# Kernel tuning notes

Hardware: AMD Instinct MI355X
Metric: run time of the kernel (lower is better)

The kernel has to match this reference:

```python
import jax, jax.numpy as jnp
import numpy as np

N = 50000
EPS = 1e-5


def gcn_conv(x, W, b, src, dst, n):
    # x: [n, Cin]; W: [Cin, Cout]; src/dst: [E+n] with self-loops included
    h = x @ W  # dense GEMM
    deg = jax.ops.segment_sum(jnp.ones_like(dst, dtype=h.dtype), dst, num_segments=n)
    dinv = jnp.where(deg > 0, jax.lax.rsqrt(deg), 0.0)
    norm = dinv[src] * dinv[dst]  # [E+n]
    msgs = h[src] * norm[:, None]  # gather + scale
    out = jax.ops.segment_sum(msgs, dst, num_segments=n)  # scatter-add
    return out + b


def batch_norm(x, gamma, beta, mean, var):
    return (x - mean) * jax.lax.rsqrt(var + EPS) * gamma + beta


def setup_inputs() -> dict:
    key = jax.random.key(0)
    ks = jax.random.split(key, 16)
    IN, H, OUT, E = 1280, 256, 500, 1600000
    x = jax.random.normal(ks[0], (N, IN), dtype=jnp.float32)
    edge_index = jax.random.randint(ks[1], (2, E), 0, N, dtype=jnp.int64)
    def lin(k, cin, cout):
        return jax.random.normal(k, (cin, cout), dtype=jnp.float32) / np.sqrt(cin)
    return {
        "x": x,
        "edge_index": edge_index,
        "W1": lin(ks[2], IN, H), "b1": jnp.zeros((H,), jnp.float32),
        "g1": jnp.ones((H,), jnp.float32), "be1": jnp.zeros((H,), jnp.float32),
        "m1": 0.1 * jax.random.normal(ks[3], (H,), jnp.float32),
        "v1": 0.5 + jax.random.uniform(ks[4], (H,), jnp.float32),
        "W2": lin(ks[5], H, H), "b2": jnp.zeros((H,), jnp.float32),
        "g2": jnp.ones((H,), jnp.float32), "be2": jnp.zeros((H,), jnp.float32),
        "m2": 0.1 * jax.random.normal(ks[6], (H,), jnp.float32),
        "v2": 0.5 + jax.random.uniform(ks[7], (H,), jnp.float32),
        "W3": lin(ks[8], H, OUT), "b3": jnp.zeros((OUT,), jnp.float32),
    }


def reference(x, edge_index, W1, b1, g1, be1, m1, v1, W2, b2, g2, be2, m2, v2, W3, b3):
    n = x.shape[0]
    loops = jnp.arange(n, dtype=edge_index.dtype)
    src = jnp.concatenate([edge_index[0], loops])
    dst = jnp.concatenate([edge_index[1], loops])
    h = gcn_conv(x, W1, b1, src, dst, n)
    h = jax.nn.relu(batch_norm(h, g1, be1, m1, v1))
    h = gcn_conv(h, W2, b2, src, dst, n)
    h = jax.nn.relu(batch_norm(h, g2, be2, m2, v2))
    return gcn_conv(h, W3, b3, src, dst, n)
```

## Files before the change

### kernel.cpp

```cpp
#include <hip/hip_runtime.h>
#include <hip/hip_bf16.h>
#include <stdint.h>

typedef __attribute__((ext_vector_type(4))) float f32x4;
typedef __attribute__((ext_vector_type(8))) short s16x8;
typedef __attribute__((ext_vector_type(4))) unsigned short u16x4;

#define EPSBN 1e-5f

__device__ __forceinline__ float bf2f(unsigned short u) {
  union { unsigned int i; float f; } w; w.i = ((unsigned int)u) << 16; return w.f;
}
__device__ __forceinline__ unsigned short f2bf(float f) {
  __hip_bfloat16 h = __float2bfloat16(f);
  unsigned short u; __builtin_memcpy(&u, &h, 2); return u;
}
__device__ __forceinline__ void gld_lds16(const void* g, void* l) {
  __builtin_amdgcn_global_load_lds(
      (const __attribute__((address_space(1))) void*)(g),
      (__attribute__((address_space(3))) void*)(l), 16, 0, 0);
}

__global__ void k_count(const int* __restrict__ dst, unsigned* __restrict__ deg, int E) {
  int i = blockIdx.x * 256 + threadIdx.x;
  if (i < E) atomicAdd(&deg[dst[i]], 1u);
}
__global__ void k_prep2(const unsigned* __restrict__ deg, float* __restrict__ dinv,
                        unsigned* __restrict__ bsum, int n) {
  __shared__ unsigned s[256];
  int t = threadIdx.x, i = blockIdx.x * 256 + t;
  unsigned d = (i < n) ? deg[i] + 1u : 0u;
  if (i < n) dinv[i] = rsqrtf((float)d);
  s[t] = d;
  __syncthreads();
  for (int st = 128; st > 0; st >>= 1) {
    if (t < st) s[t] += s[t + st];
    __syncthreads();
  }
  if (t == 0) bsum[blockIdx.x] = s[0];
}
__global__ void k_scan_top(const unsigned* __restrict__ bsum, unsigned* __restrict__ bpre,
                           int nb, unsigned* __restrict__ offs, int n) {
  __shared__ unsigned s[256];
  int t = threadIdx.x;
  unsigned v = (t < nb) ? bsum[t] : 0u;
  s[t] = v; __syncthreads();
  for (int d = 1; d < 256; d <<= 1) {
    unsigned a = (t >= d) ? s[t - d] : 0u;
    __syncthreads();
    s[t] += a;
    __syncthreads();
  }
  bpre[t] = s[t] - v;
  if (t == 255) offs[n] = s[255];
}
__global__ void k_scan_fin(const unsigned* __restrict__ deg, const unsigned* __restrict__ bpre,
                           unsigned* __restrict__ offs, unsigned* __restrict__ cur, int n) {
  __shared__ unsigned s[256];
  int t = threadIdx.x, i = blockIdx.x * 256 + t;
  unsigned v = (i < n) ? deg[i] + 1u : 0u;
  s[t] = v; __syncthreads();
  for (int d = 1; d < 256; d <<= 1) {
    unsigned a = (t >= d) ? s[t - d] : 0u;
    __syncthreads();
    s[t] += a;
    __syncthreads();
  }
  if (i < n) {
    unsigned o = bpre[blockIdx.x] + s[t] - v;
    offs[i] = o; cur[i] = o;
  }
}
__global__ void k_fill(const int* __restrict__ src, const int* __restrict__ dst,
                       unsigned* __restrict__ cur, unsigned short* __restrict__ ewp,
                       int E, int n) {
  int i = blockIdx.x * 256 + threadIdx.x;
  int s, d;
  if (i < E)          { s = src[i]; d = dst[i]; }
  else if (i < E + n) { s = d = i - E; }
  else return;
  unsigned p = atomicAdd(&cur[d], 1u);
  ewp[p] = (unsigned short)s;
}
__global__ __launch_bounds__(256) void k_sortw(const unsigned* __restrict__ offs,
                                               unsigned short* __restrict__ ewp, int nN) {
  int wv = (blockIdx.x * 256 + threadIdx.x) >> 6;
  int lane = threadIdx.x & 63;
  if (wv >= nN) return;
  unsigned beg = offs[wv], end = offs[wv + 1];
  int len = (int)(end - beg);
  if (len > 64) return;
  int k = (lane < len) ? (int)ewp[beg + lane] : 0x10000;
#pragma unroll
  for (int size = 2; size <= 64; size <<= 1) {
#pragma unroll
    for (int stride = size >> 1; stride > 0; stride >>= 1) {
      int other = __shfl_xor(k, stride);
      bool up = (lane & size) == 0;
      bool lower = (lane & stride) == 0;
      k = (lower == up) ? min(k, other) : max(k, other);
    }
  }
  if (lane < len) ewp[beg + lane] = (unsigned short)k;
}
__global__ void k_wt3(const float* __restrict__ W1, unsigned short* __restrict__ Wt1,
                      const float* __restrict__ W2, unsigned short* __restrict__ Wt2,
                      const float* __restrict__ W3, unsigned short* __restrict__ Wt3,
                      unsigned short* __restrict__ bufA, unsigned short* __restrict__ bufB,
                      int nN) {
  const int n1 = 256 * 1280, n2 = 256 * 256, n3 = 512 * 256;
  int idx = blockIdx.x * 256 + threadIdx.x;
  if (idx >= n1 + n2 + n3) {
    int z = idx - (n1 + n2 + n3);
    if (z < 256)      bufA[(size_t)nN * 256 + z] = 0;
    else if (z < 512) bufB[(size_t)nN * 256 + (z - 256)] = 0;
    return;
  }
  const float* W; unsigned short* Wt; int K, N;
  if (idx < n1)           { W = W1; Wt = Wt1; K = 1280; N = 256; }
  else if (idx < n1 + n2) { W = W2; Wt = Wt2; K = 256;  N = 256; idx -= n1; }
  else                    { W = W3; Wt = Wt3; K = 256;  N = 500; idx -= n1 + n2; }
  int nn = idx / K, k = idx - nn * K;
  float v = (nn < N) ? W[(size_t)k * N + nn] : 0.f;
  Wt[idx] = f2bf(v);
}

#define BM 128
#define BK 64

template<int OUTMODE>
__global__ __launch_bounds__(256, 4) void k_gemm(
    const unsigned short* __restrict__ Au, const unsigned short* __restrict__ Bt,
    void* __restrict__ Coutv, const float* __restrict__ bias,
    const float* __restrict__ dinv, int M, int N, int K, int MT, int NT)
{
  __shared__ __align__(16) unsigned short As[BM * BK];
  __shared__ __align__(16) unsigned short Bs[128 * BK];

  int d = blockIdx.x;
  int xc = d & 7, sb = d >> 3;
  int nt = sb % NT, mt = (sb / NT) * 8 + xc;
  if (mt >= MT) return;
  int m0 = mt * BM, n0 = nt * 128;

  int tid = threadIdx.x, lane = tid & 63, wave = tid >> 6;
  int wm = wave >> 1, wn = wave & 1;
  int l15 = lane & 15, l4 = lane >> 4;

  f32x4 acc[4][4];
#pragma unroll
  for (int i = 0; i < 4; ++i)
#pragma unroll
    for (int j = 0; j < 4; ++j) acc[i][j] = 0.f;

  int srow[4], scg[4];
#pragma unroll
  for (int i = 0; i < 4; ++i) {
    int ci = (wave + 4 * i) * 64 + lane;
    srow[i] = ci >> 3;
    scg[i] = (ci & 7) ^ (srow[i] & 7);
  }

  int nk = K / BK;
  for (int kt = 0; kt < nk; ++kt) {
    __syncthreads();
#pragma unroll
    for (int i = 0; i < 4; ++i) {
      int gr = m0 + srow[i]; gr = gr < M ? gr : M - 1;
      gld_lds16(Au + (size_t)gr * K + kt * BK + scg[i] * 8, As + (wave + 4 * i) * 512);
    }
#pragma unroll
    for (int i = 0; i < 4; ++i) {
      int gn = n0 + srow[i];
      gld_lds16(Bt + (size_t)gn * K + kt * BK + scg[i] * 8, Bs + (wave + 4 * i) * 512);
    }
    __syncthreads();

#pragma unroll
    for (int ks = 0; ks < 2; ++ks) {
      s16x8 af[4], bf[4];
#pragma unroll
      for (int f = 0; f < 4; ++f) {
        int r = wm * 64 + f * 16 + l15;
        int ca = (ks * 4 + l4) ^ (r & 7);
        af[f] = *(const s16x8*)(As + r * 64 + ca * 8);
        int nloc = wn * 64 + f * 16 + l15;
        int cb = (ks * 4 + l4) ^ (nloc & 7);
        bf[f] = *(const s16x8*)(Bs + nloc * 64 + cb * 8);
      }
#pragma unroll
      for (int fm = 0; fm < 4; ++fm)
#pragma unroll
        for (int fn = 0; fn < 4; ++fn)
          acc[fm][fn] = __builtin_amdgcn_mfma_f32_16x16x32_bf16(af[fm], bf[fn], acc[fm][fn], 0, 0, 0);
    }
  }

#pragma unroll
  for (int fm = 0; fm < 4; ++fm) {
#pragma unroll
    for (int r = 0; r < 4; ++r) {
      int row = m0 + wm * 64 + fm * 16 + l4 * 4 + r;
      float dsc = (OUTMODE == 0 && row < M) ? dinv[row] : 0.f;
#pragma unroll
      for (int fn = 0; fn < 4; ++fn) {
        int col = n0 + wn * 64 + fn * 16 + l15;
        if (row < M && col < N) {
          if (OUTMODE == 1)
            ((float*)Coutv)[(size_t)row * N + col] = acc[fm][fn][r] + bias[col];
          else
            ((unsigned short*)Coutv)[(size_t)row * N + col] = f2bf(acc[fm][fn][r] * dsc);
        }
      }
    }
  }
}

#define FBK 32
#define ASZ (BM * FBK)
#define BSZ (256 * FBK)

__global__ __launch_bounds__(512, 4) void k_gemmF(
    const float* __restrict__ Af, const unsigned short* __restrict__ Bt,
    unsigned short* __restrict__ Cout, const float* __restrict__ dinv,
    int M, int N, int K)
{
  __shared__ __align__(16) float As[2 * ASZ];
  __shared__ __align__(16) unsigned short Bs[2 * BSZ];

  int mt = blockIdx.x;
  int m0 = mt * BM;

  int tid = threadIdx.x, lane = tid & 63, wave = tid >> 6;
  int wm = wave >> 2, wn = wave & 3;
  int l15 = lane & 15, l4 = lane >> 4;

  f32x4 acc[4][4];
#pragma unroll
  for (int i = 0; i < 4; ++i)
#pragma unroll
    for (int j = 0; j < 4; ++j) acc[i][j] = 0.f;

  int arow[2], acs[2];
#pragma unroll
  for (int i = 0; i < 2; ++i) {
    int ci = i * 512 + tid;
    arow[i] = ci >> 3;
    acs[i] = (ci & 7) ^ (arow[i] & 7);
  }
  int brow[2], bcs[2];
#pragma unroll
  for (int i = 0; i < 2; ++i) {
    int ci = i * 512 + tid;
    brow[i] = ci >> 2;
    bcs[i] = (ci & 3) ^ ((brow[i] >> 1) & 3);
  }
  int gra[2];
#pragma unroll
  for (int i = 0; i < 2; ++i) {
    int gr = m0 + arow[i]; gra[i] = gr < M ? gr : M - 1;
  }

  int nk = K / FBK;
  int cur = 0;

#pragma unroll
  for (int i = 0; i < 2; ++i)
    gld_lds16(Af + (size_t)gra[i] * K + acs[i] * 4, As + (size_t)(i * 512 + wave * 64) * 4);
#pragma unroll
  for (int i = 0; i < 2; ++i)
    gld_lds16(Bt + (size_t)brow[i] * K + bcs[i] * 8, Bs + (size_t)(i * 512 + wave * 64) * 8);
  __syncthreads();

  for (int kt = 0; kt < nk; ++kt) {
    if (kt + 1 < nk) {
      int nxt = cur ^ 1;
      int kb = (kt + 1) * FBK;
#pragma unroll
      for (int i = 0; i < 2; ++i)
        gld_lds16(Af + (size_t)gra[i] * K + kb + acs[i] * 4,
                  As + (size_t)nxt * ASZ + (size_t)(i * 512 + wave * 64) * 4);
#pragma unroll
      for (int i = 0; i < 2; ++i)
        gld_lds16(Bt + (size_t)brow[i] * K + kb + bcs[i] * 8,
                  Bs + (size_t)nxt * BSZ + (size_t)(i * 512 + wave * 64) * 8);
    }
    const float* Ab = As + (size_t)cur * ASZ;
    const unsigned short* Bb = Bs + (size_t)cur * BSZ;
    s16x8 af[4], bf[4];
#pragma unroll
    for (int f = 0; f < 4; ++f) {
      int r = wm * 64 + f * 16 + l15;
      int sA = r & 7;
      int g0 = 2 * l4;
      f32x4 a0 = *(const f32x4*)(Ab + r * 32 + (g0 ^ sA) * 4);
      f32x4 a1 = *(const f32x4*)(Ab + r * 32 + ((g0 + 1) ^ sA) * 4);
      s16x8 pk;
      pk[0] = (short)f2bf(a0[0]); pk[1] = (short)f2bf(a0[1]);
      pk[2] = (short)f2bf(a0[2]); pk[3] = (short)f2bf(a0[3]);
      pk[4] = (short)f2bf(a1[0]); pk[5] = (short)f2bf(a1[1]);
      pk[6] = (short)f2bf(a1[2]); pk[7] = (short)f2bf(a1[3]);
      af[f] = pk;
      int nloc = wn * 64 + f * 16 + l15;
      int cb = l4 ^ ((nloc >> 1) & 3);
      bf[f] = *(const s16x8*)(Bb + nloc * 32 + cb * 8);
    }
#pragma unroll
    for (int fm = 0; fm < 4; ++fm)
#pragma unroll
      for (int fn = 0; fn < 4; ++fn)
        acc[fm][fn] = __builtin_amdgcn_mfma_f32_16x16x32_bf16(af[fm], bf[fn], acc[fm][fn], 0, 0, 0);
    __syncthreads();
    cur ^= 1;
  }

#pragma unroll
  for (int fm = 0; fm < 4; ++fm) {
#pragma unroll
    for (int r = 0; r < 4; ++r) {
      int row = m0 + wm * 64 + fm * 16 + l4 * 4 + r;
      float dsc = (row < M) ? dinv[row] : 0.f;
#pragma unroll
      for (int fn = 0; fn < 4; ++fn) {
        int col = wn * 64 + fn * 16 + l15;
        if (row < M && col < N)
          Cout[(size_t)row * N + col] = f2bf(acc[fm][fn][r] * dsc);
      }
    }
  }
}

template<int BNRELU, int SCALEOUT>
__global__ __launch_bounds__(256) void k_agg(
    const unsigned short* __restrict__ h, const unsigned short* __restrict__ ewp,
    const unsigned* __restrict__ offs, const float* __restrict__ dinv,
    const float* __restrict__ bias, const float* __restrict__ gam,
    const float* __restrict__ bet, const float* __restrict__ mea,
    const float* __restrict__ var, unsigned short* __restrict__ outp, int nN)
{
  int wave = threadIdx.x >> 6, lane = threadIdx.x & 63;
  int v = blockIdx.x * 4 + wave;
  if (v >= nN) return;
  unsigned beg = offs[v], end = offs[v + 1];
  int len = (int)(end - beg);
  float dv = dinv[v];
  const unsigned short* hb = h + lane * 4;
  float a0 = 0, a1 = 0, a2 = 0, a3 = 0;

  for (int base = 0; base < len; base += 64) {
    int m = min(64, len - base);
    int myp = (lane < m) ? (int)ewp[beg + base + lane] : nN;
    int ng = (m + 15) >> 4;

    u16x4 q[16];
#pragma unroll
    for (int r = 0; r < 16; ++r) {
      int s = __shfl(myp, r);
      q[r] = *(const u16x4*)(hb + (size_t)s * 256);
    }
    for (int g = 1; g < ng; ++g) {
      u16x4 q2[16];
#pragma unroll
      for (int r = 0; r < 16; ++r) {
        int s = __shfl(myp, g * 16 + r);
        q2[r] = *(const u16x4*)(hb + (size_t)s * 256);
      }
#pragma unroll
      for (int r = 0; r < 16; ++r) {
        a0 += bf2f(q[r][0]); a1 += bf2f(q[r][1]);
        a2 += bf2f(q[r][2]); a3 += bf2f(q[r][3]);
      }
#pragma unroll
      for (int r = 0; r < 16; ++r) q[r] = q2[r];
    }
#pragma unroll
    for (int r = 0; r < 16; ++r) {
      a0 += bf2f(q[r][0]); a1 += bf2f(q[r][1]);
      a2 += bf2f(q[r][2]); a3 += bf2f(q[r][3]);
    }
  }

  float va[4] = {a0, a1, a2, a3};
  int ch0 = lane * 4;
#pragma unroll
  for (int j = 0; j < 4; ++j) {
    int ch = ch0 + j;
    float val = va[j] * dv;
    if (BNRELU) {
      val += bias[ch];
      val = (val - mea[ch]) * rsqrtf(var[ch] + EPSBN) * gam[ch] + bet[ch];
      val = fmaxf(val, 0.f);
    }
    if (SCALEOUT) val *= dv;
    outp[(size_t)v * 256 + ch] = f2bf(val);
  }
}

extern "C" void kernel_launch(void* const* d_in, const int* in_sizes, int n_in,
                              void* d_out, int out_size, void* d_ws, size_t ws_size,
                              hipStream_t stream) {
  const float* x   = (const float*)d_in[0];
  const int*   ei  = (const int*)d_in[1];
  const float* W1  = (const float*)d_in[2];
  const float* b1  = (const float*)d_in[3];
  const float* g1  = (const float*)d_in[4];
  const float* be1 = (const float*)d_in[5];
  const float* m1  = (const float*)d_in[6];
  const float* v1  = (const float*)d_in[7];
  const float* W2  = (const float*)d_in[8];
  const float* b2  = (const float*)d_in[9];
  const float* g2  = (const float*)d_in[10];
  const float* be2 = (const float*)d_in[11];
  const float* m2  = (const float*)d_in[12];
  const float* v2  = (const float*)d_in[13];
  const float* W3  = (const float*)d_in[14];
  const float* b3  = (const float*)d_in[15];

  const int IN = 1280, H = 256, OUT = 500, OUTP = 512;
  int E  = in_sizes[1] / 2;
  int nN = in_sizes[0] / IN;
  const int* srcI = ei;
  const int* dstI = ei + E;

  char* p = (char*)d_ws;
  auto carve = [&](size_t bytes) { char* r = p; p += (bytes + 511) & ~(size_t)511; return r; };
  unsigned short* Wt1 = (unsigned short*)carve((size_t)H * IN * 2);
  unsigned short* Wt2 = (unsigned short*)carve((size_t)H * H * 2);
  unsigned short* Wt3 = (unsigned short*)carve((size_t)OUTP * H * 2);
  unsigned* deg  = (unsigned*)carve((size_t)nN * 4);
  float*    dinv = (float*)carve((size_t)nN * 4);
  unsigned* offs = (unsigned*)carve((size_t)(nN + 1) * 4);
  unsigned* cur  = (unsigned*)carve((size_t)nN * 4);
  unsigned* bsum = (unsigned*)carve(256 * 4);
  unsigned* bpre = (unsigned*)carve(256 * 4);
  unsigned short* ewp = (unsigned short*)carve((size_t)(E + nN) * 2);
  unsigned short* bufA = (unsigned short*)carve((size_t)(nN + 1) * H * 2);
  unsigned short* bufB = (unsigned short*)carve((size_t)(nN + 1) * H * 2);

  hipMemsetAsync(deg, 0, (size_t)nN * 4, stream);

  int NB = (nN + 255) / 256;
  k_count<<<(E + 255) / 256, 256, 0, stream>>>(dstI, deg, E);
  k_prep2<<<NB, 256, 0, stream>>>(deg, dinv, bsum, nN);
  k_scan_top<<<1, 256, 0, stream>>>(bsum, bpre, NB, offs, nN);
  k_scan_fin<<<NB, 256, 0, stream>>>(deg, bpre, offs, cur, nN);
  k_fill<<<(E + nN + 255) / 256, 256, 0, stream>>>(srcI, dstI, cur, ewp, E, nN);
  k_sortw<<<(nN + 3) / 4, 256, 0, stream>>>(offs, ewp, nN);
  k_wt3<<<(256 * 1280 + 256 * 256 + 512 * 256 + 512 + 255) / 256, 256, 0, stream>>>(
      W1, Wt1, W2, Wt2, W3, Wt3, bufA, bufB, nN);

  int MT = (nN + BM - 1) / BM;
  int mg = (MT + 7) / 8;
  int nAgg = (nN + 3) / 4;

  k_gemmF<<<MT, 512, 0, stream>>>(x, Wt1, bufA, dinv, nN, H, IN);
  k_agg<1, 0><<<nAgg, 256, 0, stream>>>(bufA, ewp, offs, dinv, b1, g1, be1, m1, v1, bufB, nN);
  k_gemm<0><<<mg * 8 * 2, 256, 0, stream>>>(bufB, Wt2, bufA, nullptr, dinv, nN, H, H, MT, 2);
  k_agg<1, 1><<<nAgg, 256, 0, stream>>>(bufA, ewp, offs, dinv, b2, g2, be2, m2, v2, bufB, nN);
  k_agg<0, 0><<<nAgg, 256, 0, stream>>>(bufB, ewp, offs, dinv, nullptr, nullptr, nullptr,
                                        nullptr, nullptr, bufA, nN);
  k_gemm<1><<<mg * 8 * 4, 256, 0, stream>>>(bufA, Wt3, d_out, b3, nullptr, nN, OUT, H, MT, 4);
}
```

Measured before the change: 682.8 us.

## Double-buffer layer-2/3 GEMM with wider tiles and vectorize aggregation stores

Replaces the 256-thread GEMM for the second and third layers with a 512-thread kernel. It uses 128x256 tiles and BK=32, and double-buffers LDS so the next tile's global-to-LDS loads overlap the MFMA work on the current tile. The XOR swizzle and the grouped block mapping are dropped, which may add LDS bank conflicts and cost L2 locality. The aggregation kernel now packs its four bf16 outputs into one nontemporal vector store and reads edge indices with nontemporal loads. Both aim to cut store instruction count and cache pollution.

```diff
diff --git a/kernel.cpp b/kernel.cpp
--- a/kernel.cpp
+++ b/kernel.cpp
@@ -126,25 +126,27 @@
 }
 
 #define BM 128
-#define BK 64
+
+#define GBK 32
+#define GASZ (BM * GBK)
+#define GBSZ (256 * GBK)
 
 template<int OUTMODE>
-__global__ __launch_bounds__(256, 4) void k_gemm(
+__global__ __launch_bounds__(512, 4) void k_gemmB(
     const unsigned short* __restrict__ Au, const unsigned short* __restrict__ Bt,
     void* __restrict__ Coutv, const float* __restrict__ bias,
-    const float* __restrict__ dinv, int M, int N, int K, int MT, int NT)
+    const float* __restrict__ dinv, int M, int N, int K, int NT)
 {
-  __shared__ __align__(16) unsigned short As[BM * BK];
-  __shared__ __align__(16) unsigned short Bs[128 * BK];
+  __shared__ __align__(16) unsigned short As[2 * GASZ];
+  __shared__ __align__(16) unsigned short Bs[2 * GBSZ];
 
   int d = blockIdx.x;
-  int xc = d & 7, sb = d >> 3;
-  int nt = sb % NT, mt = (sb / NT) * 8 + xc;
-  if (mt >= MT) return;
-  int m0 = mt * BM, n0 = nt * 128;
+  int nt = (NT == 2) ? (d & 1) : 0;
+  int mt = (NT == 2) ? (d >> 1) : d;
+  int m0 = mt * BM, n0 = nt * 256;
 
   int tid = threadIdx.x, lane = tid & 63, wave = tid >> 6;
-  int wm = wave >> 1, wn = wave & 1;
+  int wm = wave >> 2, wn = wave & 3;
   int l15 = lane & 15, l4 = lane >> 4;
 
   f32x4 acc[4][4];
@@ -153,47 +155,53 @@
 #pragma unroll
     for (int j = 0; j < 4; ++j) acc[i][j] = 0.f;
 
-  int srow[4], scg[4];
-#pragma unroll
-  for (int i = 0; i < 4; ++i) {
-    int ci = (wave + 4 * i) * 64 + lane;
-    srow[i] = ci >> 3;
-    scg[i] = (ci & 7) ^ (srow[i] & 7);
-  }
-
-  int nk = K / BK;
+  int ar = tid >> 2, ac = tid & 3;
+  int gra = m0 + ar; gra = gra < M ? gra : M - 1;
+  int br[2], bc[2];
+#pragma unroll
+  for (int i = 0; i < 2; ++i) {
+    int ci = i * 512 + tid;
+    br[i] = ci >> 2; bc[i] = ci & 3;
+  }
+
+  int nk = K / GBK;
+  int cur = 0;
+
+  gld_lds16(Au + (size_t)gra * K + ac * 8, As + (size_t)(wave * 64) * 8);
+#pragma unroll
+  for (int i = 0; i < 2; ++i)
+    gld_lds16(Bt + (size_t)(n0 + br[i]) * K + bc[i] * 8,
+              Bs + (size_t)(i * 512 + wave * 64) * 8);
+  __syncthreads();
+
   for (int kt = 0; kt < nk; ++kt) {
-    __syncthreads();
-#pragma unroll
-    for (int i = 0; i < 4; ++i) {
-      int gr = m0 + srow[i]; gr = gr < M ? gr : M - 1;
-      gld_lds16(Au + (size_t)gr * K + kt * BK + scg[i] * 8, As + (wave + 4 * i) * 512);
-    }
-#pragma unroll
-    for (int i = 0; i < 4; ++i) {
-      int gn = n0 + srow[i];
-      gld_lds16(Bt + (size_t)gn * K + kt * BK + scg[i] * 8, Bs + (wave + 4 * i) * 512);
-    }
-    __syncthreads();
-
-#pragma unroll
-    for (int ks = 0; ks < 2; ++ks) {
-      s16x8 af[4], bf[4];
-#pragma unroll
-      for (int f = 0; f < 4; ++f) {
-        int r = wm * 64 + f * 16 + l15;
-        int ca = (ks * 4 + l4) ^ (r & 7);
-        af[f] = *(const s16x8*)(As + r * 64 + ca * 8);
-        int nloc = wn * 64 + f * 16 + l15;
-        int cb = (ks * 4 + l4) ^ (nloc & 7);
-        bf[f] = *(const s16x8*)(Bs + nloc * 64 + cb * 8);
-      }
-#pragma unroll
-      for (int fm = 0; fm < 4; ++fm)
-#pragma unroll
-        for (int fn = 0; fn < 4; ++fn)
-          acc[fm][fn] = __builtin_amdgcn_mfma_f32_16x16x32_bf16(af[fm], bf[fn], acc[fm][fn], 0, 0, 0);
-    }
+    if (kt + 1 < nk) {
+      int nxt = cur ^ 1;
+      int kb = (kt + 1) * GBK;
+      gld_lds16(Au + (size_t)gra * K + kb + ac * 8,
+                As + (size_t)nxt * GASZ + (size_t)(wave * 64) * 8);
+#pragma unroll
+      for (int i = 0; i < 2; ++i)
+        gld_lds16(Bt + (size_t)(n0 + br[i]) * K + kb + bc[i] * 8,
+                  Bs + (size_t)nxt * GBSZ + (size_t)(i * 512 + wave * 64) * 8);
+    }
+    const unsigned short* Ab = As + (size_t)cur * GASZ;
+    const unsigned short* Bb = Bs + (size_t)cur * GBSZ;
+    s16x8 af[4], bf[4];
+#pragma unroll
+    for (int f = 0; f < 4; ++f) {
+      int r = wm * 64 + f * 16 + l15;
+      af[f] = *(const s16x8*)(Ab + r * 32 + l4 * 8);
+      int nloc = wn * 64 + f * 16 + l15;
+      bf[f] = *(const s16x8*)(Bb + nloc * 32 + l4 * 8);
+    }
+#pragma unroll
+    for (int fm = 0; fm < 4; ++fm)
+#pragma unroll
+      for (int fn = 0; fn < 4; ++fn)
+        acc[fm][fn] = __builtin_amdgcn_mfma_f32_16x16x32_bf16(af[fm], bf[fn], acc[fm][fn], 0, 0, 0);
+    __syncthreads();
+    cur ^= 1;
   }
 
 #pragma unroll
@@ -349,7 +357,7 @@
 
   for (int base = 0; base < len; base += 64) {
     int m = min(64, len - base);
-    int myp = (lane < m) ? (int)ewp[beg + base + lane] : nN;
+    int myp = (lane < m) ? (int)__builtin_nontemporal_load(&ewp[beg + base + lane]) : nN;
     int ng = (m + 15) >> 4;
 
     u16x4 q[16];
@@ -382,6 +390,7 @@
 
   float va[4] = {a0, a1, a2, a3};
   int ch0 = lane * 4;
+  u16x4 o;
 #pragma unroll
   for (int j = 0; j < 4; ++j) {
     int ch = ch0 + j;
@@ -392,8 +401,9 @@
       val = fmaxf(val, 0.f);
     }
     if (SCALEOUT) val *= dv;
-    outp[(size_t)v * 256 + ch] = f2bf(val);
-  }
+    o[j] = f2bf(val);
+  }
+  __builtin_nontemporal_store(o, (u16x4*)(outp + (size_t)v * 256 + ch0));
 }
 
 extern "C" void kernel_launch(void* const* d_in, const int* in_sizes, int n_in,
@@ -450,14 +460,13 @@
       W1, Wt1, W2, Wt2, W3, Wt3, bufA, bufB, nN);
 
   int MT = (nN + BM - 1) / BM;
-  int mg = (MT + 7) / 8;
   int nAgg = (nN + 3) / 4;
 
   k_gemmF<<<MT, 512, 0, stream>>>(x, Wt1, bufA, dinv, nN, H, IN);
   k_agg<1, 0><<<nAgg, 256, 0, stream>>>(bufA, ewp, offs, dinv, b1, g1, be1, m1, v1, bufB, nN);
-  k_gemm<0><<<mg * 8 * 2, 256, 0, stream>>>(bufB, Wt2, bufA, nullptr, dinv, nN, H, H, MT, 2);
+  k_gemmB<0><<<MT, 512, 0, stream>>>(bufB, Wt2, bufA, nullptr, dinv, nN, H, H, 1);
   k_agg<1, 1><<<nAgg, 256, 0, stream>>>(bufA, ewp, offs, dinv, b2, g2, be2, m2, v2, bufB, nN);
   k_agg<0, 0><<<nAgg, 256, 0, stream>>>(bufB, ewp, offs, dinv, nullptr, nullptr, nullptr,
                                         nullptr, nullptr, bufA, nN);
-  k_gemm<1><<<mg * 8 * 4, 256, 0, stream>>>(bufA, Wt3, d_out, b3, nullptr, nN, OUT, H, MT, 4);
-}
+  k_gemmB<1><<<MT * 2, 512, 0, stream>>>(bufA, Wt3, d_out, b3, nullptr, nN, OUT, H, 2);
+}
```

Result: slower. 696.8 us (+2.0%).
